# Kernel optimization log

Measured on AMD Instinct MI355X. Metric: run time of the kernel, lower is better.

Reference implementation:

```python
import jax, jax.numpy as jnp
import numpy as np

HEADS = 16
DIM_HEAD = 64
SCALE = DIM_HEAD ** -0.5
LN_EPS = 1e-5


def setup_inputs() -> dict:
    key = jax.random.key(0)
    k1, k2, k3 = jax.random.split(key, 3)
    b, s, d = 2, 2048, 1024
    inner = HEADS * DIM_HEAD
    x = jax.random.normal(k1, (b, s, d), dtype=jnp.float32)
    w_qkv = jax.random.normal(k2, (d, 3 * inner), dtype=jnp.float32) * (d ** -0.5)
    w_out = jax.random.normal(k3, (inner, d), dtype=jnp.float32) * (inner ** -0.5)
    return {
        "x": x,
        "ln_gamma": jnp.ones((d,), jnp.float32),
        "ln_beta": jnp.zeros((d,), jnp.float32),
        "w_qkv": w_qkv,
        "w_out": w_out,
        "b_out": jnp.zeros((d,), jnp.float32),
    }


def _layernorm(x, gamma, beta):
    mu = jnp.mean(x, axis=-1, keepdims=True)
    var = jnp.var(x, axis=-1, keepdims=True)
    return (x - mu) * jax.lax.rsqrt(var + LN_EPS) * gamma + beta


def reference(x, ln_gamma, ln_beta, w_qkv, w_out, b_out):
    b, s, d = x.shape
    xn = _layernorm(x, ln_gamma, ln_beta)
    qkv = xn @ w_qkv                       # [b, s, 3*inner]
    q, k, v = jnp.split(qkv, 3, axis=-1)
    def heads(t):
        return t.reshape(b, s, HEADS, DIM_HEAD).transpose(0, 2, 1, 3)  # [b, h, s, dh]
    q, k, v = heads(q), heads(k), heads(v)
    dots = jnp.einsum("bhqd,bhkd->bhqk", q, k) * SCALE   # [b, h, s, s]
    attn = jax.nn.softmax(dots, axis=-1)
    out = jnp.einsum("bhqk,bhkd->bhqd", attn, v)          # [b, h, s, dh]
    out = out.transpose(0, 2, 1, 3).reshape(b, s, HEADS * DIM_HEAD)
    return out @ w_out + b_out
```

## Files before the change

### kernel.cpp

```cpp
#include <hip/hip_runtime.h>
#include <hip/hip_bf16.h>
#include <stdint.h>

#define NH     16
#define DHEAD  64
#define SEQ    2048
#define DMODEL 1024
#define NBATCH 2
#define INNER  1024
#define QKVN   3072
#define ROWS   4096
#define ATT_QB 128
#define ATT_KB 64
#define KSPLIT 2

typedef __attribute__((ext_vector_type(8))) __bf16 bf16x8;
typedef __attribute__((ext_vector_type(4))) float floatx4;

__device__ __forceinline__ unsigned short f2bf(float f) {
    union { __bf16 b; unsigned short u; } c; c.b = (__bf16)f; return c.u;
}

typedef __attribute__((address_space(1))) void gvoid;
typedef __attribute__((address_space(3))) void lvoid;
__device__ __forceinline__ void gl_lds16(const void* g, void* l) {
    __builtin_amdgcn_global_load_lds((gvoid*)g, (lvoid*)l, 16, 0, 0);
}

__global__ __launch_bounds__(256) void transpose_f2b(
        const float* __restrict__ in, unsigned short* __restrict__ out,
        int rows, int cols) {
    __shared__ unsigned short tile[32][33];
    const int bx = blockIdx.x * 32, by = blockIdx.y * 32;
    const int tx = threadIdx.x & 31, ty = threadIdx.x >> 5;
    for (int i = ty; i < 32; i += 8)
        tile[i][tx] = f2bf(in[(size_t)(by + i) * cols + bx + tx]);
    __syncthreads();
    for (int i = ty; i < 32; i += 8)
        out[(size_t)(bx + i) * rows + by + tx] = tile[tx][i];
}

__global__ __launch_bounds__(256) void ln_kernel(
        const float* __restrict__ x,
        const float* __restrict__ gamma,
        const float* __restrict__ beta,
        unsigned short* __restrict__ xn) {
    __shared__ float red[4][2];
    const int row = blockIdx.x, t = threadIdx.x;
    const size_t base = (size_t)row * DMODEL + t * 4;
    float4 v = *(const float4*)(x + base);
    float s  = v.x + v.y + v.z + v.w;
    float ss = v.x*v.x + v.y*v.y + v.z*v.z + v.w*v.w;
    for (int off = 32; off >= 1; off >>= 1) {
        s  += __shfl_xor(s,  off);
        ss += __shfl_xor(ss, off);
    }
    const int w = t >> 6, lane = t & 63;
    if (lane == 0) { red[w][0] = s; red[w][1] = ss; }
    __syncthreads();
    if (t == 0) {
        float S  = red[0][0] + red[1][0] + red[2][0] + red[3][0];
        float SS = red[0][1] + red[1][1] + red[2][1] + red[3][1];
        float mu  = S * (1.f / DMODEL);
        float var = SS * (1.f / DMODEL) - mu * mu;
        red[0][0] = mu; red[0][1] = rsqrtf(var + 1e-5f);
    }
    __syncthreads();
    const float mu = red[0][0], rstd = red[0][1];
    float4 g = *(const float4*)(gamma + t * 4);
    float4 bb = *(const float4*)(beta + t * 4);
    ushort4 o;
    o.x = f2bf((v.x - mu) * rstd * g.x + bb.x);
    o.y = f2bf((v.y - mu) * rstd * g.y + bb.y);
    o.z = f2bf((v.z - mu) * rstd * g.z + bb.z);
    o.w = f2bf((v.w - mu) * rstd * g.w + bb.w);
    *(ushort4*)(xn + base) = o;
}

__global__ __launch_bounds__(256) void gemm_qkv(
        const unsigned short* __restrict__ A,
        const unsigned short* __restrict__ Bt,
        unsigned short* __restrict__ qP,
        unsigned short* __restrict__ kP,
        unsigned short* __restrict__ vT) {
    const int K = DMODEL;
    __shared__ __align__(16) unsigned short sA[128 * 32];
    __shared__ __align__(16) unsigned short sB[128 * 32];
    __shared__ __align__(16) unsigned short tb[2][64 * 72];
    const int t = threadIdx.x;
    const int mBase = blockIdx.y * 128, nBase = blockIdx.x * 128;
    const int w = t >> 6, lane = t & 63, quad = lane >> 4, l16 = lane & 15;
    const int wm = (w >> 1) * 64, wn = (w & 1) * 64;
    const int srow = t >> 2, sch = t & 3;
    floatx4 acc[4][4];
    for (int mi = 0; mi < 4; mi++)
        for (int ni = 0; ni < 4; ni++) acc[mi][ni] = (floatx4)0.f;

    for (int k0 = 0; k0 < K; k0 += 32) {
        #pragma unroll
        for (int c = 0; c < 2; c++) {
            const int row = c * 64 + srow;
            const int gcol = (sch ^ ((row >> 1) & 3)) * 8;
            gl_lds16(&A[(size_t)(mBase + row) * K + k0 + gcol], &sA[(c * 256 + w * 64) * 8]);
            gl_lds16(&Bt[(size_t)(nBase + row) * K + k0 + gcol], &sB[(c * 256 + w * 64) * 8]);
        }
        __syncthreads();
        bf16x8 af[4], bfv[4];
        #pragma unroll
        for (int mi = 0; mi < 4; mi++) {
            const int r = wm + mi * 16 + l16;
            af[mi] = *(const bf16x8*)&sA[r * 32 + (quad ^ ((r >> 1) & 3)) * 8];
        }
        #pragma unroll
        for (int ni = 0; ni < 4; ni++) {
            const int r = wn + ni * 16 + l16;
            bfv[ni] = *(const bf16x8*)&sB[r * 32 + (quad ^ ((r >> 1) & 3)) * 8];
        }
        #pragma unroll
        for (int mi = 0; mi < 4; mi++)
            #pragma unroll
            for (int ni = 0; ni < 4; ni++)
                acc[mi][ni] = __builtin_amdgcn_mfma_f32_16x16x32_bf16(
                    af[mi], bfv[ni], acc[mi][ni], 0, 0, 0);
        __syncthreads();
    }
    const int reg = nBase >> 10;
    if (reg == 2) {
        #pragma unroll
        for (int ni = 0; ni < 4; ni++) {
            const int col = nBase + wn + ni * 16 + l16;
            const int h = (col & 1023) >> 6, dh = col & 63;
            #pragma unroll
            for (int mi = 0; mi < 4; mi++) {
                const int row0 = mBase + wm + mi * 16 + quad * 4;
                const int b = row0 >> 11, s0 = row0 & 2047;
                ushort4 o;
                o.x = f2bf(acc[mi][ni][0]); o.y = f2bf(acc[mi][ni][1]);
                o.z = f2bf(acc[mi][ni][2]); o.w = f2bf(acc[mi][ni][3]);
                *(ushort4*)&vT[((size_t)(b * NH + h) * DHEAD + dh) * SEQ + s0] = o;
            }
        }
    } else {
        unsigned short* dst = (reg == 0) ? qP : kP;
        const float scl = (reg == 0) ? 0.125f : 1.f;
        const int hh = ((nBase + wn) & 1023) >> 6;
        #pragma unroll
        for (int ph = 0; ph < 2; ph++) {
            if ((w >> 1) == ph) {
                unsigned short* tb_ = &tb[w & 1][0];
                #pragma unroll
                for (int mi = 0; mi < 4; mi++)
                    #pragma unroll
                    for (int ni = 0; ni < 4; ni++)
                        #pragma unroll
                        for (int i = 0; i < 4; i++)
                            tb_[(mi * 16 + quad * 4 + i) * 72 + ni * 16 + l16] =
                                f2bf(acc[mi][ni][i] * scl);
                asm volatile("s_waitcnt lgkmcnt(0)" ::: "memory");
                const int row_g = mBase + wm + lane;
                const int b = row_g >> 11, sr = row_g & 2047;
                unsigned short* orow = dst + ((size_t)(b * NH + hh) * SEQ + sr) * DHEAD;
                #pragma unroll
                for (int c = 0; c < 8; c++)
                    *(bf16x8*)&orow[c * 8] = *(const bf16x8*)&tb_[lane * 72 + c * 8];
            }
            __syncthreads();
        }
    }
}

__global__ __launch_bounds__(256) void gemm_out(
        const unsigned short* __restrict__ A,
        const unsigned short* __restrict__ Bt,
        float* __restrict__ C,
        const int M, const int N, const int K,
        const float* __restrict__ bias) {
    __shared__ __align__(16) unsigned short sA[128 * 32];
    __shared__ __align__(16) unsigned short sB[64 * 32];
    const int t = threadIdx.x;
    const int mBase = blockIdx.y * 128, nBase = blockIdx.x * 64;
    const int w = t >> 6, lane = t & 63, quad = lane >> 4, l16 = lane & 15;
    const int wm = (w >> 1) * 64, wn = (w & 1) * 32;
    const int srow = t >> 2, sch = t & 3;
    floatx4 acc[4][2];
    for (int mi = 0; mi < 4; mi++)
        for (int ni = 0; ni < 2; ni++) acc[mi][ni] = (floatx4)0.f;

    for (int k0 = 0; k0 < K; k0 += 32) {
        #pragma unroll
        for (int c = 0; c < 2; c++) {
            const int row = c * 64 + srow;
            const int gcol = (sch ^ ((row >> 1) & 3)) * 8;
            gl_lds16(&A[(size_t)(mBase + row) * K + k0 + gcol], &sA[(c * 256 + w * 64) * 8]);
        }
        {
            const int gcol = (sch ^ ((srow >> 1) & 3)) * 8;
            gl_lds16(&Bt[(size_t)(nBase + srow) * K + k0 + gcol], &sB[(w * 64) * 8]);
        }
        __syncthreads();
        bf16x8 af[4], bfv[2];
        #pragma unroll
        for (int mi = 0; mi < 4; mi++) {
            const int r = wm + mi * 16 + l16;
            af[mi] = *(const bf16x8*)&sA[r * 32 + (quad ^ ((r >> 1) & 3)) * 8];
        }
        #pragma unroll
        for (int ni = 0; ni < 2; ni++) {
            const int r = wn + ni * 16 + l16;
            bfv[ni] = *(const bf16x8*)&sB[r * 32 + (quad ^ ((r >> 1) & 3)) * 8];
        }
        #pragma unroll
        for (int mi = 0; mi < 4; mi++)
            #pragma unroll
            for (int ni = 0; ni < 2; ni++)
                acc[mi][ni] = __builtin_amdgcn_mfma_f32_16x16x32_bf16(
                    af[mi], bfv[ni], acc[mi][ni], 0, 0, 0);
        __syncthreads();
    }
    #pragma unroll
    for (int mi = 0; mi < 4; mi++)
        #pragma unroll
        for (int ni = 0; ni < 2; ni++) {
            const int col = nBase + wn + ni * 16 + l16;
            const float badd = bias ? bias[col] : 0.f;
            #pragma unroll
            for (int i = 0; i < 4; i++) {
                const int row = mBase + wm + mi * 16 + quad * 4 + i;
                C[(size_t)row * N + col] = acc[mi][ni][i] + badd;
            }
        }
}

__global__ __launch_bounds__(256) void attn_kernel(
        const unsigned short* __restrict__ qP,
        const unsigned short* __restrict__ kP,
        const unsigned short* __restrict__ vT,
        float* __restrict__ Opart,
        float* __restrict__ lpart) {
    __shared__ __align__(16) unsigned short sK[2][ATT_KB * 64];
    __shared__ __align__(16) unsigned short sV[2][ATT_KB * 64];
    __shared__ __align__(16) unsigned short sP[4][2][16 * 64];
    const int t = threadIdx.x, w = t >> 6, lane = t & 63;
    const int quad = lane >> 4, l16 = lane & 15;
    const int bh = blockIdx.y, b = bh >> 4, h = bh & 15;
    const int z = blockIdx.z;
    const int kvBase = z * (SEQ / KSPLIT);
    const int qbase = blockIdx.x * ATT_QB + w * 32;
    const int swr = l16 & 7;

    bf16x8 aq[2][2];
    #pragma unroll
    for (int st = 0; st < 2; st++)
        #pragma unroll
        for (int hh = 0; hh < 2; hh++)
            aq[st][hh] = *(const bf16x8*)&qP[
                ((size_t)bh * SEQ + qbase + st * 16 + l16) * DHEAD + hh * 32 + quad * 8];

    floatx4 oac[2][4];
    float lS[2] = {0.f, 0.f};
    #pragma unroll
    for (int st = 0; st < 2; st++)
        #pragma unroll
        for (int c = 0; c < 4; c++) oac[st][c] = (floatx4)0.f;

    const unsigned short* kb = kP + (size_t)bh * SEQ * DHEAD;
    const unsigned short* vb = vT + (size_t)bh * DHEAD * SEQ;
    const int r8 = lane >> 3, sw8 = ((lane & 7) ^ r8) * 8;

    auto stage = [&](int it, int bi) {
        const int kv0 = kvBase + it * ATT_KB;
        #pragma unroll
        for (int ii = 0; ii < 2; ii++) {
            const int row = w * 16 + ii * 8 + r8;
            gl_lds16(kb + (size_t)(kv0 + row) * DHEAD + sw8,
                     (void*)&sK[bi][(w * 16 + ii * 8) * 64]);
            gl_lds16(vb + (size_t)row * SEQ + kv0 + sw8,
                     (void*)&sV[bi][(w * 16 + ii * 8) * 64]);
        }
    };
    stage(0, 0);

    const int NIT = SEQ / KSPLIT / ATT_KB;
    for (int it = 0; it < NIT; ++it) {
        __syncthreads();
        if (it + 1 < NIT) stage(it + 1, (it + 1) & 1);
        const unsigned short* sKb = &sK[it & 1][0];
        const unsigned short* sVb = &sV[it & 1][0];

        bf16x8 kf[4][2];
        #pragma unroll
        for (int c = 0; c < 4; c++)
            #pragma unroll
            for (int hh = 0; hh < 2; hh++)
                kf[c][hh] = *(const bf16x8*)&sKb[(c * 16 + l16) * 64 +
                                                 8 * (((hh << 2) | quad) ^ swr)];
        floatx4 sv[2][4];
        #pragma unroll
        for (int st = 0; st < 2; st++)
            #pragma unroll
            for (int c = 0; c < 4; c++) {
                floatx4 a = (floatx4)0.f;
                a = __builtin_amdgcn_mfma_f32_16x16x32_bf16(kf[c][0], aq[st][0], a, 0, 0, 0);
                a = __builtin_amdgcn_mfma_f32_16x16x32_bf16(kf[c][1], aq[st][1], a, 0, 0, 0);
                sv[st][c] = a;
            }
        #pragma unroll
        for (int st = 0; st < 2; st++) {
            float sum = 0.f;
            unsigned short* pb = (unsigned short*)&sP[w][st][0];
            #pragma unroll
            for (int c = 0; c < 4; c++) {
                float p0 = __expf(sv[st][c][0]), p1 = __expf(sv[st][c][1]);
                float p2 = __expf(sv[st][c][2]), p3 = __expf(sv[st][c][3]);
                sum += (p0 + p1) + (p2 + p3);
                ushort4 pk;
                pk.x = f2bf(p0); pk.y = f2bf(p1); pk.z = f2bf(p2); pk.w = f2bf(p3);
                *(ushort4*)&pb[l16 * 64 + 8 * ((((c << 1) | (quad >> 1))) ^ swr) + (quad & 1) * 4] = pk;
            }
            sum += __shfl_xor(sum, 16);
            sum += __shfl_xor(sum, 32);
            lS[st] += sum;
        }
        bf16x8 vf[4][2];
        #pragma unroll
        for (int c = 0; c < 4; c++)
            #pragma unroll
            for (int hh = 0; hh < 2; hh++)
                vf[c][hh] = *(const bf16x8*)&sVb[(c * 16 + l16) * 64 +
                                                 8 * (((hh << 2) | quad) ^ swr)];
        asm volatile("s_waitcnt lgkmcnt(0)" ::: "memory");
        #pragma unroll
        for (int st = 0; st < 2; st++) {
            const unsigned short* pb = (const unsigned short*)&sP[w][st][0];
            bf16x8 pf[2];
            #pragma unroll
            for (int hh = 0; hh < 2; hh++)
                pf[hh] = *(const bf16x8*)&pb[l16 * 64 + 8 * (((hh << 2) | quad) ^ swr)];
            #pragma unroll
            for (int c = 0; c < 4; c++) {
                oac[st][c] = __builtin_amdgcn_mfma_f32_16x16x32_bf16(vf[c][0], pf[0], oac[st][c], 0, 0, 0);
                oac[st][c] = __builtin_amdgcn_mfma_f32_16x16x32_bf16(vf[c][1], pf[1], oac[st][c], 0, 0, 0);
            }
        }
    }
    float* Ob = Opart + (size_t)z * ROWS * INNER;
    #pragma unroll
    for (int st = 0; st < 2; st++) {
        const size_t rb = (size_t)(b * SEQ + qbase + st * 16 + l16) * INNER + h * DHEAD;
        #pragma unroll
        for (int c = 0; c < 4; c++) {
            float4 o;
            o.x = oac[st][c][0]; o.y = oac[st][c][1];
            o.z = oac[st][c][2]; o.w = oac[st][c][3];
            *(float4*)&Ob[rb + c * 16 + quad * 4] = o;
        }
    }
    if (quad == 0) {
        #pragma unroll
        for (int st = 0; st < 2; st++)
            lpart[((size_t)z * NBATCH * NH + bh) * SEQ + qbase + st * 16 + l16] = lS[st];
    }
}

__global__ __launch_bounds__(256) void attn_combine(
        const float* __restrict__ Opart,
        const float* __restrict__ lpart,
        unsigned short* __restrict__ aout) {
    const int row = blockIdx.x, t = threadIdx.x;
    const int b = row >> 11, s = row & 2047;
    __shared__ float rls[16];
    if (t < 16) {
        const size_t i0 = ((size_t)(b * NH + t)) * SEQ + s;
        rls[t] = 1.f / (lpart[i0] + lpart[(size_t)NBATCH * NH * SEQ + i0]);
    }
    __syncthreads();
    const size_t base = (size_t)row * INNER + t * 4;
    float4 o0 = *(const float4*)(Opart + base);
    float4 o1 = *(const float4*)(Opart + (size_t)ROWS * INNER + base);
    const float rl = rls[t >> 4];
    ushort4 o;
    o.x = f2bf((o0.x + o1.x) * rl);
    o.y = f2bf((o0.y + o1.y) * rl);
    o.z = f2bf((o0.z + o1.z) * rl);
    o.w = f2bf((o0.w + o1.w) * rl);
    *(ushort4*)&aout[base] = o;
}

extern "C" void kernel_launch(void* const* d_in, const int* in_sizes, int n_in,
                              void* d_out, int out_size, void* d_ws, size_t ws_size,
                              hipStream_t stream) {
    const float* x     = (const float*)d_in[0];
    const float* gamma = (const float*)d_in[1];
    const float* beta  = (const float*)d_in[2];
    const float* wqkv  = (const float*)d_in[3];
    const float* wout  = (const float*)d_in[4];
    const float* bout  = (const float*)d_in[5];
    float* out = (float*)d_out;

    unsigned short* ws     = (unsigned short*)d_ws;
    unsigned short* xn     = ws;
    unsigned short* wqkvT  = xn     + (size_t)ROWS * DMODEL;
    unsigned short* qPb    = wqkvT  + (size_t)QKVN * DMODEL;
    unsigned short* kPb    = qPb    + (size_t)NBATCH * NH * SEQ * DHEAD;
    unsigned short* vTb    = kPb    + (size_t)NBATCH * NH * SEQ * DHEAD;
    unsigned short* attnO  = vTb    + (size_t)NBATCH * NH * SEQ * DHEAD;
    unsigned short* woutT  = attnO  + (size_t)ROWS * INNER;
    float* Opart = (float*)(woutT + (size_t)DMODEL * INNER);
    float* lpart = Opart + (size_t)KSPLIT * ROWS * INNER;

    transpose_f2b<<<dim3(QKVN / 32, DMODEL / 32), 256, 0, stream>>>(wqkv, wqkvT, DMODEL, QKVN);
    transpose_f2b<<<dim3(DMODEL / 32, INNER / 32), 256, 0, stream>>>(wout, woutT, INNER, DMODEL);
    ln_kernel<<<ROWS, 256, 0, stream>>>(x, gamma, beta, xn);
    gemm_qkv<<<dim3(QKVN / 128, ROWS / 128), 256, 0, stream>>>(xn, wqkvT, qPb, kPb, vTb);
    attn_kernel<<<dim3(SEQ / ATT_QB, NBATCH * NH, KSPLIT), 256, 0, stream>>>(
        qPb, kPb, vTb, Opart, lpart);
    attn_combine<<<ROWS, 256, 0, stream>>>(Opart, lpart, attnO);
    gemm_out<<<dim3(DMODEL / 64, ROWS / 128), 256, 0, stream>>>(
        attnO, woutT, out, ROWS, DMODEL, INNER, bout);
}
```

Measured before the change: 226.3 us.

## Fuse split-KV combine into output GEMM and merge prep kernels into one launch

Merges layernorm and both weight transpose/convert kernels into a single prep launch that dispatches on block index. It removes the attn_combine kernel: the output GEMM now reads both fp32 partial attention outputs, sums them, scales by the reciprocal softmax denominator and converts to bf16 while staging the A tile into LDS. The output GEMM tile also grows from 128x64 to 128x128. This drops the bf16 intermediate round trip and two launches, at the cost of synchronous fp32 register loads for A (no async global-to-LDS copy) and half as many GEMM blocks.

```diff
diff --git a/kernel.cpp b/kernel.cpp
--- a/kernel.cpp
+++ b/kernel.cpp
@@ -27,54 +27,66 @@
     __builtin_amdgcn_global_load_lds((gvoid*)g, (lvoid*)l, 16, 0, 0);
 }
 
-__global__ __launch_bounds__(256) void transpose_f2b(
-        const float* __restrict__ in, unsigned short* __restrict__ out,
-        int rows, int cols) {
-    __shared__ unsigned short tile[32][33];
-    const int bx = blockIdx.x * 32, by = blockIdx.y * 32;
-    const int tx = threadIdx.x & 31, ty = threadIdx.x >> 5;
-    for (int i = ty; i < 32; i += 8)
-        tile[i][tx] = f2bf(in[(size_t)(by + i) * cols + bx + tx]);
-    __syncthreads();
-    for (int i = ty; i < 32; i += 8)
-        out[(size_t)(bx + i) * rows + by + tx] = tile[tx][i];
-}
-
-__global__ __launch_bounds__(256) void ln_kernel(
+__global__ __launch_bounds__(256) void prep_kernel(
         const float* __restrict__ x,
         const float* __restrict__ gamma,
         const float* __restrict__ beta,
-        unsigned short* __restrict__ xn) {
+        const float* __restrict__ wqkv,
+        const float* __restrict__ wout,
+        unsigned short* __restrict__ xn,
+        unsigned short* __restrict__ wqkvT,
+        unsigned short* __restrict__ woutT) {
+    __shared__ unsigned short tile[32][33];
     __shared__ float red[4][2];
-    const int row = blockIdx.x, t = threadIdx.x;
-    const size_t base = (size_t)row * DMODEL + t * 4;
-    float4 v = *(const float4*)(x + base);
-    float s  = v.x + v.y + v.z + v.w;
-    float ss = v.x*v.x + v.y*v.y + v.z*v.z + v.w*v.w;
-    for (int off = 32; off >= 1; off >>= 1) {
-        s  += __shfl_xor(s,  off);
-        ss += __shfl_xor(ss, off);
-    }
-    const int w = t >> 6, lane = t & 63;
-    if (lane == 0) { red[w][0] = s; red[w][1] = ss; }
-    __syncthreads();
-    if (t == 0) {
-        float S  = red[0][0] + red[1][0] + red[2][0] + red[3][0];
-        float SS = red[0][1] + red[1][1] + red[2][1] + red[3][1];
-        float mu  = S * (1.f / DMODEL);
-        float var = SS * (1.f / DMODEL) - mu * mu;
-        red[0][0] = mu; red[0][1] = rsqrtf(var + 1e-5f);
-    }
-    __syncthreads();
-    const float mu = red[0][0], rstd = red[0][1];
-    float4 g = *(const float4*)(gamma + t * 4);
-    float4 bb = *(const float4*)(beta + t * 4);
-    ushort4 o;
-    o.x = f2bf((v.x - mu) * rstd * g.x + bb.x);
-    o.y = f2bf((v.y - mu) * rstd * g.y + bb.y);
-    o.z = f2bf((v.z - mu) * rstd * g.z + bb.z);
-    o.w = f2bf((v.w - mu) * rstd * g.w + bb.w);
-    *(ushort4*)(xn + base) = o;
+    const int bid = blockIdx.x, t = threadIdx.x;
+    if (bid < ROWS) {
+        const size_t base = (size_t)bid * DMODEL + t * 4;
+        float4 v = *(const float4*)(x + base);
+        float s  = v.x + v.y + v.z + v.w;
+        float ss = v.x*v.x + v.y*v.y + v.z*v.z + v.w*v.w;
+        for (int off = 32; off >= 1; off >>= 1) {
+            s  += __shfl_xor(s,  off);
+            ss += __shfl_xor(ss, off);
+        }
+        const int w = t >> 6, lane = t & 63;
+        if (lane == 0) { red[w][0] = s; red[w][1] = ss; }
+        __syncthreads();
+        if (t == 0) {
+            float S  = red[0][0] + red[1][0] + red[2][0] + red[3][0];
+            float SS = red[0][1] + red[1][1] + red[2][1] + red[3][1];
+            float mu  = S * (1.f / DMODEL);
+            float var = SS * (1.f / DMODEL) - mu * mu;
+            red[0][0] = mu; red[0][1] = rsqrtf(var + 1e-5f);
+        }
+        __syncthreads();
+        const float mu = red[0][0], rstd = red[0][1];
+        float4 g = *(const float4*)(gamma + t * 4);
+        float4 bb = *(const float4*)(beta + t * 4);
+        ushort4 o;
+        o.x = f2bf((v.x - mu) * rstd * g.x + bb.x);
+        o.y = f2bf((v.y - mu) * rstd * g.y + bb.y);
+        o.z = f2bf((v.z - mu) * rstd * g.z + bb.z);
+        o.w = f2bf((v.w - mu) * rstd * g.w + bb.w);
+        *(ushort4*)(xn + base) = o;
+    } else if (bid < ROWS + (QKVN / 32) * (DMODEL / 32)) {
+        const int tid = bid - ROWS;
+        const int bx = (tid % (QKVN / 32)) * 32, by = (tid / (QKVN / 32)) * 32;
+        const int tx = t & 31, ty = t >> 5;
+        for (int i = ty; i < 32; i += 8)
+            tile[i][tx] = f2bf(wqkv[(size_t)(by + i) * QKVN + bx + tx]);
+        __syncthreads();
+        for (int i = ty; i < 32; i += 8)
+            wqkvT[(size_t)(bx + i) * DMODEL + by + tx] = tile[tx][i];
+    } else {
+        const int tid = bid - ROWS - (QKVN / 32) * (DMODEL / 32);
+        const int bx = (tid & 31) * 32, by = (tid >> 5) * 32;
+        const int tx = t & 31, ty = t >> 5;
+        for (int i = ty; i < 32; i += 8)
+            tile[i][tx] = f2bf(wout[(size_t)(by + i) * DMODEL + bx + tx]);
+        __syncthreads();
+        for (int i = ty; i < 32; i += 8)
+            woutT[(size_t)(bx + i) * INNER + by + tx] = tile[tx][i];
+    }
 }
 
 __global__ __launch_bounds__(256) void gemm_qkv(
@@ -169,68 +181,6 @@
     }
 }
 
-__global__ __launch_bounds__(256) void gemm_out(
-        const unsigned short* __restrict__ A,
-        const unsigned short* __restrict__ Bt,
-        float* __restrict__ C,
-        const int M, const int N, const int K,
-        const float* __restrict__ bias) {
-    __shared__ __align__(16) unsigned short sA[128 * 32];
-    __shared__ __align__(16) unsigned short sB[64 * 32];
-    const int t = threadIdx.x;
-    const int mBase = blockIdx.y * 128, nBase = blockIdx.x * 64;
-    const int w = t >> 6, lane = t & 63, quad = lane >> 4, l16 = lane & 15;
-    const int wm = (w >> 1) * 64, wn = (w & 1) * 32;
-    const int srow = t >> 2, sch = t & 3;
-    floatx4 acc[4][2];
-    for (int mi = 0; mi < 4; mi++)
-        for (int ni = 0; ni < 2; ni++) acc[mi][ni] = (floatx4)0.f;
-
-    for (int k0 = 0; k0 < K; k0 += 32) {
-        #pragma unroll
-        for (int c = 0; c < 2; c++) {
-            const int row = c * 64 + srow;
-            const int gcol = (sch ^ ((row >> 1) & 3)) * 8;
-            gl_lds16(&A[(size_t)(mBase + row) * K + k0 + gcol], &sA[(c * 256 + w * 64) * 8]);
-        }
-        {
-            const int gcol = (sch ^ ((srow >> 1) & 3)) * 8;
-            gl_lds16(&Bt[(size_t)(nBase + srow) * K + k0 + gcol], &sB[(w * 64) * 8]);
-        }
-        __syncthreads();
-        bf16x8 af[4], bfv[2];
-        #pragma unroll
-        for (int mi = 0; mi < 4; mi++) {
-            const int r = wm + mi * 16 + l16;
-            af[mi] = *(const bf16x8*)&sA[r * 32 + (quad ^ ((r >> 1) & 3)) * 8];
-        }
-        #pragma unroll
-        for (int ni = 0; ni < 2; ni++) {
-            const int r = wn + ni * 16 + l16;
-            bfv[ni] = *(const bf16x8*)&sB[r * 32 + (quad ^ ((r >> 1) & 3)) * 8];
-        }
-        #pragma unroll
-        for (int mi = 0; mi < 4; mi++)
-            #pragma unroll
-            for (int ni = 0; ni < 2; ni++)
-                acc[mi][ni] = __builtin_amdgcn_mfma_f32_16x16x32_bf16(
-                    af[mi], bfv[ni], acc[mi][ni], 0, 0, 0);
-        __syncthreads();
-    }
-    #pragma unroll
-    for (int mi = 0; mi < 4; mi++)
-        #pragma unroll
-        for (int ni = 0; ni < 2; ni++) {
-            const int col = nBase + wn + ni * 16 + l16;
-            const float badd = bias ? bias[col] : 0.f;
-            #pragma unroll
-            for (int i = 0; i < 4; i++) {
-                const int row = mBase + wm + mi * 16 + quad * 4 + i;
-                C[(size_t)row * N + col] = acc[mi][ni][i] + badd;
-            }
-        }
-}
-
 __global__ __launch_bounds__(256) void attn_kernel(
         const unsigned short* __restrict__ qP,
         const unsigned short* __restrict__ kP,
@@ -362,28 +312,92 @@
     }
 }
 
-__global__ __launch_bounds__(256) void attn_combine(
+__global__ __launch_bounds__(256) void gemm_out_fused(
         const float* __restrict__ Opart,
         const float* __restrict__ lpart,
-        unsigned short* __restrict__ aout) {
-    const int row = blockIdx.x, t = threadIdx.x;
-    const int b = row >> 11, s = row & 2047;
-    __shared__ float rls[16];
-    if (t < 16) {
-        const size_t i0 = ((size_t)(b * NH + t)) * SEQ + s;
-        rls[t] = 1.f / (lpart[i0] + lpart[(size_t)NBATCH * NH * SEQ + i0]);
+        const unsigned short* __restrict__ Bt,
+        const float* __restrict__ bias,
+        float* __restrict__ C) {
+    const int N = DMODEL, K = INNER;
+    __shared__ __align__(16) unsigned short sA[128 * 32];
+    __shared__ __align__(16) unsigned short sB[128 * 32];
+    __shared__ float rls[NH * 128];
+    const int t = threadIdx.x;
+    const int mBase = blockIdx.y * 128, nBase = blockIdx.x * 128;
+    const int w = t >> 6, lane = t & 63, quad = lane >> 4, l16 = lane & 15;
+    const int wm = (w >> 1) * 64, wn = (w & 1) * 64;
+    const int srow = t >> 2, sch = t & 3;
+    #pragma unroll
+    for (int j = 0; j < 8; j++) {
+        const int e = t * 8 + j;
+        const int h = e >> 7, r = e & 127;
+        const int row = mBase + r, b = row >> 11, s = row & 2047;
+        const size_t li = (size_t)(b * NH + h) * SEQ + s;
+        rls[e] = 1.f / (lpart[li] + lpart[(size_t)KSPLIT / 2 * NBATCH * NH * SEQ + li]);
     }
     __syncthreads();
-    const size_t base = (size_t)row * INNER + t * 4;
-    float4 o0 = *(const float4*)(Opart + base);
-    float4 o1 = *(const float4*)(Opart + (size_t)ROWS * INNER + base);
-    const float rl = rls[t >> 4];
-    ushort4 o;
-    o.x = f2bf((o0.x + o1.x) * rl);
-    o.y = f2bf((o0.y + o1.y) * rl);
-    o.z = f2bf((o0.z + o1.z) * rl);
-    o.w = f2bf((o0.w + o1.w) * rl);
-    *(ushort4*)&aout[base] = o;
+    floatx4 acc[4][4];
+    for (int mi = 0; mi < 4; mi++)
+        for (int ni = 0; ni < 4; ni++) acc[mi][ni] = (floatx4)0.f;
+
+    for (int k0 = 0; k0 < K; k0 += 32) {
+        const float* rh = &rls[(k0 >> 6) * 128];
+        #pragma unroll
+        for (int c = 0; c < 2; c++) {
+            const int ci = c * 256 + t;
+            const int r = ci >> 2, ch = ci & 3;
+            const int gc = ch ^ ((r >> 1) & 3);
+            const float* p0 = Opart + (size_t)(mBase + r) * INNER + k0 + gc * 8;
+            const float* p1 = p0 + (size_t)ROWS * INNER;
+            float4 a0 = *(const float4*)p0, a1 = *(const float4*)(p0 + 4);
+            float4 b0 = *(const float4*)p1, b1 = *(const float4*)(p1 + 4);
+            const float rl = rh[r];
+            union { unsigned short u[8]; bf16x8 v; } pk;
+            pk.u[0] = f2bf((a0.x + b0.x) * rl);
+            pk.u[1] = f2bf((a0.y + b0.y) * rl);
+            pk.u[2] = f2bf((a0.z + b0.z) * rl);
+            pk.u[3] = f2bf((a0.w + b0.w) * rl);
+            pk.u[4] = f2bf((a1.x + b1.x) * rl);
+            pk.u[5] = f2bf((a1.y + b1.y) * rl);
+            pk.u[6] = f2bf((a1.z + b1.z) * rl);
+            pk.u[7] = f2bf((a1.w + b1.w) * rl);
+            *(bf16x8*)&sA[r * 32 + ch * 8] = pk.v;
+            const int rowb = c * 64 + srow;
+            const int gcol = (sch ^ ((rowb >> 1) & 3)) * 8;
+            gl_lds16(&Bt[(size_t)(nBase + rowb) * K + k0 + gcol], &sB[(c * 256 + w * 64) * 8]);
+        }
+        __syncthreads();
+        bf16x8 af[4], bfv[4];
+        #pragma unroll
+        for (int mi = 0; mi < 4; mi++) {
+            const int r = wm + mi * 16 + l16;
+            af[mi] = *(const bf16x8*)&sA[r * 32 + (quad ^ ((r >> 1) & 3)) * 8];
+        }
+        #pragma unroll
+        for (int ni = 0; ni < 4; ni++) {
+            const int r = wn + ni * 16 + l16;
+            bfv[ni] = *(const bf16x8*)&sB[r * 32 + (quad ^ ((r >> 1) & 3)) * 8];
+        }
+        #pragma unroll
+        for (int mi = 0; mi < 4; mi++)
+            #pragma unroll
+            for (int ni = 0; ni < 4; ni++)
+                acc[mi][ni] = __builtin_amdgcn_mfma_f32_16x16x32_bf16(
+                    af[mi], bfv[ni], acc[mi][ni], 0, 0, 0);
+        __syncthreads();
+    }
+    #pragma unroll
+    for (int mi = 0; mi < 4; mi++)
+        #pragma unroll
+        for (int ni = 0; ni < 4; ni++) {
+            const int col = nBase + wn + ni * 16 + l16;
+            const float badd = bias[col];
+            #pragma unroll
+            for (int i = 0; i < 4; i++) {
+                const int row = mBase + wm + mi * 16 + quad * 4 + i;
+                C[(size_t)row * N + col] = acc[mi][ni][i] + badd;
+            }
+        }
 }
 
 extern "C" void kernel_launch(void* const* d_in, const int* in_sizes, int n_in,
@@ -403,18 +417,15 @@
     unsigned short* qPb    = wqkvT  + (size_t)QKVN * DMODEL;
     unsigned short* kPb    = qPb    + (size_t)NBATCH * NH * SEQ * DHEAD;
     unsigned short* vTb    = kPb    + (size_t)NBATCH * NH * SEQ * DHEAD;
-    unsigned short* attnO  = vTb    + (size_t)NBATCH * NH * SEQ * DHEAD;
-    unsigned short* woutT  = attnO  + (size_t)ROWS * INNER;
+    unsigned short* woutT  = vTb    + (size_t)NBATCH * NH * SEQ * DHEAD;
     float* Opart = (float*)(woutT + (size_t)DMODEL * INNER);
     float* lpart = Opart + (size_t)KSPLIT * ROWS * INNER;
 
-    transpose_f2b<<<dim3(QKVN / 32, DMODEL / 32), 256, 0, stream>>>(wqkv, wqkvT, DMODEL, QKVN);
-    transpose_f2b<<<dim3(DMODEL / 32, INNER / 32), 256, 0, stream>>>(wout, woutT, INNER, DMODEL);
-    ln_kernel<<<ROWS, 256, 0, stream>>>(x, gamma, beta, xn);
+    const int PREP_BLKS = ROWS + (QKVN / 32) * (DMODEL / 32) + (DMODEL / 32) * (INNER / 32);
+    prep_kernel<<<PREP_BLKS, 256, 0, stream>>>(x, gamma, beta, wqkv, wout, xn, wqkvT, woutT);
     gemm_qkv<<<dim3(QKVN / 128, ROWS / 128), 256, 0, stream>>>(xn, wqkvT, qPb, kPb, vTb);
     attn_kernel<<<dim3(SEQ / ATT_QB, NBATCH * NH, KSPLIT), 256, 0, stream>>>(
         qPb, kPb, vTb, Opart, lpart);
-    attn_combine<<<ROWS, 256, 0, stream>>>(Opart, lpart, attnO);
-    gemm_out<<<dim3(DMODEL / 64, ROWS / 128), 256, 0, stream>>>(
-        attnO, woutT, out, ROWS, DMODEL, INNER, bout);
-}
+    gemm_out_fused<<<dim3(DMODEL / 128, ROWS / 128), 256, 0, stream>>>(
+        Opart, lpart, woutT, bout, out);
+}
```

Result: slower. 239.3 us (+5.7%).
